# Optimization experiments

Hardware: AMD Instinct MI355X
Metric: run time of the kernel (lower is better)

## Reference

```python
import jax, jax.numpy as jnp
import numpy as np

MAX_SET_SIZE = 8


def setup_inputs() -> dict:
    key = jax.random.key(0)
    ks = jax.random.split(key, 8)
    n_items, L, d_v = 8192, 64, 128
    n_chains, hidden = 32768, 128
    v = jax.random.normal(ks[0], (n_items, L, d_v), dtype=jnp.float32)
    batch_idx = jax.random.randint(ks[1], (n_chains,), 0, n_items, dtype=jnp.int32)
    mask = jax.random.randint(ks[2], (n_chains, L), 0, 2) > 0
    count = jax.random.randint(ks[3], (n_chains,), 0, 64, dtype=jnp.int32)
    in_dim = MAX_SET_SIZE * d_v + 1
    W1 = jax.random.normal(ks[4], (in_dim, hidden), dtype=jnp.float32) / np.sqrt(in_dim)
    b1 = jnp.zeros((hidden,), dtype=jnp.float32)
    W2 = jax.random.normal(ks[5], (hidden, d_v), dtype=jnp.float32) / np.sqrt(hidden)
    b2 = jnp.zeros((d_v,), dtype=jnp.float32)
    return {"v": v, "batch_idx": batch_idx, "mask": mask, "count": count,
            "W1": W1, "b1": b1, "W2": W2, "b2": b2}


def reference(v, batch_idx, mask, count, W1, b1, W2, b2):
    n_chains, L = mask.shape
    d_v = v.shape[-1]
    K = MAX_SET_SIZE  # k_keep = min(max_set_size, L) = 8 since L >= 8
    # score = mask * (L - pos): earlier positions score higher; top_k picks
    # the first K masked positions (ties impossible among masked entries).
    pos = jnp.arange(L, dtype=jnp.float32)
    scores = mask.astype(jnp.float32) * (jnp.float32(L) - pos)[None, :]
    top_scores, top_idx = jax.lax.top_k(scores, K)        # [n_chains, K]
    picked = top_scores > 0
    sortable = jnp.where(picked, top_idx, L)              # sentinel L for unpicked
    order = jnp.argsort(sortable, axis=1)                 # restore index order
    sortable = jnp.take_along_axis(sortable, order, axis=1)
    picked = jnp.take_along_axis(picked, order, axis=1)
    safe_idx = jnp.where(picked, sortable, 0)
    # Fused gather: v[batch_idx[c], safe_idx[c, k], :] -> [n_chains, K, d_v]
    packed = v[batch_idx[:, None], safe_idx]
    packed = packed * picked[..., None].astype(v.dtype)
    flat = packed.reshape(n_chains, K * d_v)
    log_count = jnp.log1p(count.astype(v.dtype))[:, None]
    x = jnp.concatenate([flat, log_count], axis=-1)       # [n_chains, K*d_v + 1]
    h = jax.nn.gelu(x @ W1 + b1, approximate=False)       # exact GELU (torch default)
    return h @ W2 + b2
```

## Files before the change

### kernel.cpp

```cpp
#include <hip/hip_runtime.h>
#include <hip/hip_bf16.h>
#include <math.h>


typedef __attribute__((ext_vector_type(8))) short bf16x8;
typedef __attribute__((ext_vector_type(4))) float f32x4;

#define NCHAINS 32768
#define LPOS    64
#define DV      128
#define HID     128
#define KDIM    1024
#define CPB     32

__device__ __forceinline__ unsigned short cvt_bf16(float a) {
  unsigned u = __float_as_uint(a);
  u += 0x7fffu + ((u >> 16) & 1u);
  return (unsigned short)(u >> 16);
}
__device__ __forceinline__ unsigned pk2_bf16(float a, float b) {
  unsigned ua = __float_as_uint(a), ub = __float_as_uint(b);
  ua += 0x7fffu + ((ua >> 16) & 1u);
  ub += 0x7fffu + ((ub >> 16) & 1u);
  return (ua >> 16) | (ub & 0xffff0000u);
}
__device__ __forceinline__ bf16x8 pack8(float4 a, float4 b) {
  union { bf16x8 v; unsigned u[4]; } r;
  r.u[0] = pk2_bf16(a.x, a.y);
  r.u[1] = pk2_bf16(a.z, a.w);
  r.u[2] = pk2_bf16(b.x, b.y);
  r.u[3] = pk2_bf16(b.z, b.w);
  return r.v;
}
__device__ __forceinline__ float gelu_exact(float x) {
  return 0.5f * x * (1.0f + erff(x * 0.70710678118654752f));
}

__global__ __launch_bounds__(256) void prep_kernel(
    const float* __restrict__ W1, const float* __restrict__ W2,
    unsigned short* __restrict__ W1p, unsigned short* __restrict__ W2p,
    float* __restrict__ zr) {
  int id = blockIdx.x * 256 + threadIdx.x;
  {
    int j = id & 7, lx = (id >> 3) & 63, nt = (id >> 9) & 7, ch = id >> 12;
    int k = ch * 32 + ((lx >> 4) & 3) * 8 + j;
    int n = nt * 16 + (lx & 15);
    W1p[id] = cvt_bf16(W1[k * HID + n]);
    if (id < 16384) {
      int ch2 = id >> 12;
      int k2 = ch2 * 32 + ((lx >> 4) & 3) * 8 + j;
      W2p[id] = cvt_bf16(W2[k2 * HID + n]);
    }
  }
  if (id < DV) zr[id] = 0.0f;
}

__global__ __launch_bounds__(256, 5) void agg_mlp_kernel(
    const float* __restrict__ v, const int* __restrict__ batch_idx,
    const int* __restrict__ mask, const int* __restrict__ count,
    const float* __restrict__ W1, const float* __restrict__ b1,
    const float* __restrict__ b2,
    const unsigned short* __restrict__ W1p, const unsigned short* __restrict__ W2p,
    const float* __restrict__ zr, float* __restrict__ out) {
  __shared__ const float* s_ptr[CPB][8];
  __shared__ float s_logc[CPB];
  __shared__ unsigned short s_H[CPB][HID + 8];

  const int tid = threadIdx.x;
  const int blk = blockIdx.x;

  if (tid < CPB) {
    int c = blk * CPB + tid;
    const int4* mp = (const int4*)(mask + (size_t)c * LPOS);
    unsigned long long m64 = 0;
    #pragma unroll
    for (int q = 0; q < 16; q++) {
      int4 mm = mp[q];
      unsigned long long b = (mm.x != 0 ? 1ull : 0ull) | (mm.y != 0 ? 2ull : 0ull) |
                             (mm.z != 0 ? 4ull : 0ull) | (mm.w != 0 ? 8ull : 0ull);
      m64 |= b << (q * 4);
    }
    const float* base = v + (size_t)batch_idx[c] * (LPOS * DV);
    #pragma unroll
    for (int s = 0; s < 8; s++) {
      const float* p;
      if (m64) {
        int pos = __ffsll(m64) - 1;
        m64 &= (m64 - 1);
        p = base + pos * DV;
      } else {
        p = zr;
      }
      s_ptr[tid][s] = p;
    }
    s_logc[tid] = log1pf((float)count[c]);
  }
  __syncthreads();

  const int l = tid & 63, w = tid >> 6;
  const int mh = w & 1, cb = w >> 1;
  const int m = l & 15, kq = l >> 4;
  const int chain = mh * 16 + m;

  f32x4 acc0 = {0.f,0.f,0.f,0.f}, acc1 = {0.f,0.f,0.f,0.f};
  f32x4 acc2 = {0.f,0.f,0.f,0.f}, acc3 = {0.f,0.f,0.f,0.f};

  #pragma unroll 2
  for (int ch = 0; ch < 32; ch++) {
    const int s = ch >> 2, q = ch & 3;
    const float* pa = s_ptr[chain][s] + q * 32 + kq * 8;
    float4 x0 = *(const float4*)pa;
    float4 x1 = *(const float4*)(pa + 4);
    const unsigned short* wb = W1p + ((size_t)(ch * 8 + cb * 4) * 64 + l) * 8;
    bf16x8 b0 = *(const bf16x8*)(wb);
    bf16x8 b1f = *(const bf16x8*)(wb + 512);
    bf16x8 b2f = *(const bf16x8*)(wb + 1024);
    bf16x8 b3f = *(const bf16x8*)(wb + 1536);
    bf16x8 a = pack8(x0, x1);
    acc0 = __builtin_amdgcn_mfma_f32_16x16x32_bf16(a, b0,  acc0, 0, 0, 0);
    acc1 = __builtin_amdgcn_mfma_f32_16x16x32_bf16(a, b1f, acc1, 0, 0, 0);
    acc2 = __builtin_amdgcn_mfma_f32_16x16x32_bf16(a, b2f, acc2, 0, 0, 0);
    acc3 = __builtin_amdgcn_mfma_f32_16x16x32_bf16(a, b3f, acc3, 0, 0, 0);
  }

  {
    float w1l[4], b1v[4];
    #pragma unroll
    for (int nt = 0; nt < 4; nt++) {
      int n = cb * 64 + nt * 16 + m;
      w1l[nt] = W1[KDIM * HID + n];
      b1v[nt] = b1[n];
    }
    f32x4* accs[4] = {&acc0, &acc1, &acc2, &acc3};
    #pragma unroll
    for (int r = 0; r < 4; r++) {
      int row = mh * 16 + kq * 4 + r;
      float lc = s_logc[row];
      #pragma unroll
      for (int nt = 0; nt < 4; nt++) {
        float h = (*accs[nt])[r] + lc * w1l[nt] + b1v[nt];
        s_H[row][cb * 64 + nt * 16 + m] = cvt_bf16(gelu_exact(h));
      }
    }
  }
  __syncthreads();

  f32x4 d0 = {0.f,0.f,0.f,0.f}, d1 = {0.f,0.f,0.f,0.f};
  f32x4 d2 = {0.f,0.f,0.f,0.f}, d3 = {0.f,0.f,0.f,0.f};

  #pragma unroll
  for (int ch = 0; ch < 4; ch++) {
    bf16x8 a = *(const bf16x8*)&s_H[mh * 16 + m][ch * 32 + kq * 8];
    const unsigned short* wb = W2p + ((size_t)(ch * 8 + cb * 4) * 64 + l) * 8;
    bf16x8 b0 = *(const bf16x8*)(wb);
    bf16x8 b1f = *(const bf16x8*)(wb + 512);
    bf16x8 b2f = *(const bf16x8*)(wb + 1024);
    bf16x8 b3f = *(const bf16x8*)(wb + 1536);
    d0 = __builtin_amdgcn_mfma_f32_16x16x32_bf16(a, b0,  d0, 0, 0, 0);
    d1 = __builtin_amdgcn_mfma_f32_16x16x32_bf16(a, b1f, d1, 0, 0, 0);
    d2 = __builtin_amdgcn_mfma_f32_16x16x32_bf16(a, b2f, d2, 0, 0, 0);
    d3 = __builtin_amdgcn_mfma_f32_16x16x32_bf16(a, b3f, d3, 0, 0, 0);
  }

  {
    float b2v[4];
    #pragma unroll
    for (int nt = 0; nt < 4; nt++) b2v[nt] = b2[cb * 64 + nt * 16 + m];
    f32x4* ds[4] = {&d0, &d1, &d2, &d3};
    #pragma unroll
    for (int r = 0; r < 4; r++) {
      int row = mh * 16 + kq * 4 + r;
      size_t o = (size_t)(blk * CPB + row) * DV;
      #pragma unroll
      for (int nt = 0; nt < 4; nt++) {
        out[o + cb * 64 + nt * 16 + m] = (*ds[nt])[r] + b2v[nt];
      }
    }
  }
}

extern "C" void kernel_launch(void* const* d_in, const int* in_sizes, int n_in,
                              void* d_out, int out_size, void* d_ws, size_t ws_size,
                              hipStream_t stream) {
  const float* v          = (const float*)d_in[0];
  const int* batch_idx    = (const int*)d_in[1];
  const int* mk           = (const int*)d_in[2];
  const int* count        = (const int*)d_in[3];
  const float* W1         = (const float*)d_in[4];
  const float* b1         = (const float*)d_in[5];
  const float* W2         = (const float*)d_in[6];
  const float* b2         = (const float*)d_in[7];
  float* out              = (float*)d_out;

  char* ws = (char*)d_ws;
  unsigned short* W1p = (unsigned short*)ws;
  unsigned short* W2p = (unsigned short*)(ws + 262144);
  float* zr           = (float*)(ws + 262144 + 32768);

  prep_kernel<<<512, 256, 0, stream>>>(W1, W2, W1p, W2p, zr);
  agg_mlp_kernel<<<NCHAINS / CPB, 256, 0, stream>>>(
      v, batch_idx, mk, count, W1, b1, b2, W1p, W2p, zr, out);
}
```

Baseline: 373.6 us.

## Split gather into separate bf16 pack kernel writing MFMA-ready layout

Moves the masked gather and fp32-to-bf16 conversion out of the fused MLP kernel into a dedicated kernel. That kernel writes a pre-swizzled bf16 activation buffer (64 MB) in MFMA fragment order, so the GEMM kernel streams contiguous coalesced bf16x8 loads instead of scattered fp32 row reads. Each half of the work can then run at its own occupancy. In exchange it adds a full write and re-read of the intermediate buffer through global memory, plus an extra launch.

```diff
diff --git a/kernel.cpp b/kernel.cpp
--- a/kernel.cpp
+++ b/kernel.cpp
@@ -23,14 +23,6 @@
   ua += 0x7fffu + ((ua >> 16) & 1u);
   ub += 0x7fffu + ((ub >> 16) & 1u);
   return (ua >> 16) | (ub & 0xffff0000u);
-}
-__device__ __forceinline__ bf16x8 pack8(float4 a, float4 b) {
-  union { bf16x8 v; unsigned u[4]; } r;
-  r.u[0] = pk2_bf16(a.x, a.y);
-  r.u[1] = pk2_bf16(a.z, a.w);
-  r.u[2] = pk2_bf16(b.x, b.y);
-  r.u[3] = pk2_bf16(b.z, b.w);
-  return r.v;
 }
 __device__ __forceinline__ float gelu_exact(float x) {
   return 0.5f * x * (1.0f + erff(x * 0.70710678118654752f));
@@ -55,22 +47,17 @@
   if (id < DV) zr[id] = 0.0f;
 }
 
-__global__ __launch_bounds__(256, 5) void agg_mlp_kernel(
+__global__ __launch_bounds__(256, 8) void gather_pack_kernel(
     const float* __restrict__ v, const int* __restrict__ batch_idx,
-    const int* __restrict__ mask, const int* __restrict__ count,
-    const float* __restrict__ W1, const float* __restrict__ b1,
-    const float* __restrict__ b2,
-    const unsigned short* __restrict__ W1p, const unsigned short* __restrict__ W2p,
-    const float* __restrict__ zr, float* __restrict__ out) {
-  __shared__ const float* s_ptr[CPB][8];
-  __shared__ float s_logc[CPB];
-  __shared__ unsigned short s_H[CPB][HID + 8];
+    const int* __restrict__ mask,
+    const float* __restrict__ zr, unsigned short* __restrict__ Xp) {
+  __shared__ const float* s_rp[16][8];
 
   const int tid = threadIdx.x;
-  const int blk = blockIdx.x;
-
-  if (tid < CPB) {
-    int c = blk * CPB + tid;
+  const int ht = blockIdx.x;
+
+  if (tid < 16) {
+    int c = ht * 16 + tid;
     const int4* mp = (const int4*)(mask + (size_t)c * LPOS);
     unsigned long long m64 = 0;
     #pragma unroll
@@ -91,32 +78,69 @@
       } else {
         p = zr;
       }
-      s_ptr[tid][s] = p;
-    }
-    s_logc[tid] = log1pf((float)count[c]);
-  }
+      s_rp[tid][s] = p;
+    }
+  }
+  __syncthreads();
+
+  const int w = tid >> 6, l = tid & 63;
+  const int m = l >> 2, kq = l & 3;
+  const int g = w * 64 + ((l >> 2) | ((l & 3) << 4));
+  const int koff = w * 32 + kq * 8;
+
+  const float* p[8];
+  #pragma unroll
+  for (int s = 0; s < 8; s++) p[s] = s_rp[m][s];
+
+  uint4* dst = (uint4*)(Xp + (size_t)ht * 16384) + g;
+
+  #pragma unroll
+  for (int i = 0; i < 8; i++) {
+    const float* src = p[i] + koff;
+    float4 x0 = *(const float4*)src;
+    float4 x1 = *(const float4*)(src + 4);
+    uint4 o;
+    o.x = pk2_bf16(x0.x, x0.y);
+    o.y = pk2_bf16(x0.z, x0.w);
+    o.z = pk2_bf16(x1.x, x1.y);
+    o.w = pk2_bf16(x1.z, x1.w);
+    dst[i * 256] = o;
+  }
+}
+
+__global__ __launch_bounds__(256, 4) void gemm_kernel(
+    const int* __restrict__ count,
+    const float* __restrict__ W1, const float* __restrict__ b1,
+    const float* __restrict__ b2,
+    const unsigned short* __restrict__ W1p, const unsigned short* __restrict__ W2p,
+    const unsigned short* __restrict__ Xp, float* __restrict__ out) {
+  __shared__ float s_logc[CPB];
+  __shared__ unsigned short s_H[CPB][HID + 8];
+
+  const int tid = threadIdx.x;
+  const int blk = blockIdx.x;
+
+  if (tid < CPB) s_logc[tid] = log1pf((float)count[blk * CPB + tid]);
   __syncthreads();
 
   const int l = tid & 63, w = tid >> 6;
   const int mh = w & 1, cb = w >> 1;
   const int m = l & 15, kq = l >> 4;
-  const int chain = mh * 16 + m;
+
+  const unsigned short* ap = Xp + (size_t)(2 * blk + mh) * 16384 + l * 8;
+  const unsigned short* bp = W1p + ((size_t)(cb * 4) * 64 + l) * 8;
 
   f32x4 acc0 = {0.f,0.f,0.f,0.f}, acc1 = {0.f,0.f,0.f,0.f};
   f32x4 acc2 = {0.f,0.f,0.f,0.f}, acc3 = {0.f,0.f,0.f,0.f};
 
   #pragma unroll 2
   for (int ch = 0; ch < 32; ch++) {
-    const int s = ch >> 2, q = ch & 3;
-    const float* pa = s_ptr[chain][s] + q * 32 + kq * 8;
-    float4 x0 = *(const float4*)pa;
-    float4 x1 = *(const float4*)(pa + 4);
-    const unsigned short* wb = W1p + ((size_t)(ch * 8 + cb * 4) * 64 + l) * 8;
+    bf16x8 a = *(const bf16x8*)(ap + (size_t)ch * 512);
+    const unsigned short* wb = bp + (size_t)ch * 4096;
     bf16x8 b0 = *(const bf16x8*)(wb);
     bf16x8 b1f = *(const bf16x8*)(wb + 512);
     bf16x8 b2f = *(const bf16x8*)(wb + 1024);
     bf16x8 b3f = *(const bf16x8*)(wb + 1536);
-    bf16x8 a = pack8(x0, x1);
     acc0 = __builtin_amdgcn_mfma_f32_16x16x32_bf16(a, b0,  acc0, 0, 0, 0);
     acc1 = __builtin_amdgcn_mfma_f32_16x16x32_bf16(a, b1f, acc1, 0, 0, 0);
     acc2 = __builtin_amdgcn_mfma_f32_16x16x32_bf16(a, b2f, acc2, 0, 0, 0);
@@ -196,8 +220,10 @@
   unsigned short* W1p = (unsigned short*)ws;
   unsigned short* W2p = (unsigned short*)(ws + 262144);
   float* zr           = (float*)(ws + 262144 + 32768);
+  unsigned short* Xp  = (unsigned short*)(ws + 262144 + 32768 + 512);
 
   prep_kernel<<<512, 256, 0, stream>>>(W1, W2, W1p, W2p, zr);
-  agg_mlp_kernel<<<NCHAINS / CPB, 256, 0, stream>>>(
-      v, batch_idx, mk, count, W1, b1, b2, W1p, W2p, zr, out);
-}
+  gather_pack_kernel<<<NCHAINS / 16, 256, 0, stream>>>(v, batch_idx, mk, zr, Xp);
+  gemm_kernel<<<NCHAINS / CPB, 256, 0, stream>>>(
+      count, W1, b1, b2, W1p, W2p, Xp, out);
+}
```

New measurement: 373.6 us. No clear change (-0.0%).
